# Kernel optimization log

Hardware: AMD Instinct MI355X
Metric: run time of the kernel (lower is better)

The kernel has to match this reference:

```python
import jax, jax.numpy as jnp
import numpy as np

B = 16384
D = 64            # bottom_mlp_layers[-1] = embedding_dim
DENSE = 512
HIST = 50         # history length per row
C_CAMP = 1000     # num_collisions for campaign table (sqrt(1e6))
C_FEAT = 316      # num_collisions for 1e5-vocab tables
NQ_CAMP = 1000    # ceil(1e6/1000)
NQ_FEAT = 317     # ceil(1e5/316)
NFEAT = 7
N = NFEAT + 1 + 1 # sparse features + dense row
PROJ = 128


def setup_inputs() -> dict:
    key = jax.random.key(0)
    ks = jax.random.split(key, 20)
    inp = {
        'x': jax.random.normal(ks[0], (B, DENSE), jnp.float32),
        'hist_idx': jax.random.randint(ks[1], (B * HIST,), 0, 1000000),
        'hist_offsets': jnp.arange(B, dtype=jnp.int64) * HIST,
        'feat_idx': jax.random.randint(ks[2], (B, NFEAT), 0, 100000),
        # QR embedding tables (quotient, remainder)
        'Wq_c': jax.random.normal(ks[3], (NQ_CAMP, D), jnp.float32) * 0.05,
        'Wr_c': jax.random.normal(ks[4], (C_CAMP, D), jnp.float32) * 0.05,
        'Wq_f': jax.random.normal(ks[5], (NFEAT, NQ_FEAT, D), jnp.float32) * 0.05,
        'Wr_f': jax.random.normal(ks[6], (NFEAT, C_FEAT, D), jnp.float32) * 0.05,
        # bottom MLP: 512->512 relu 512->256 relu 256->64
        'W0': jax.random.normal(ks[7], (512, DENSE), jnp.float32) * 0.03,
        'b0': jnp.zeros((512,), jnp.float32),
        'W1': jax.random.normal(ks[8], (256, 512), jnp.float32) * 0.04,
        'b1': jnp.zeros((256,), jnp.float32),
        'W2': jax.random.normal(ks[9], (64, 256), jnp.float32) * 0.06,
        'b2': jnp.zeros((64,), jnp.float32),
        # projection: (D + (N^2-N)/2) -> PROJ ; 64 + 36 = 100
        'Wp': jax.random.normal(ks[10], (PROJ, D + (N * N - N) // 2), jnp.float32) * 0.1,
        'bp': jnp.zeros((PROJ,), jnp.float32),
    }
    return inp


def _forward(x, hist_idx, hist_offsets, feat_idx, Wq_c, Wr_c, Wq_f, Wr_f,
             W0, b0, W1, b1, W2, b2, Wp, bp):
    # bottom MLP
    h = jax.nn.relu(x @ W0.T + b0)
    h = jax.nn.relu(h @ W1.T + b1)
    dense = h @ W2.T + b2                                   # [B, D]

    # QR embedding bag (mode='mean', operation='mult') for history feature
    e = Wq_c[hist_idx // C_CAMP] * Wr_c[hist_idx % C_CAMP]  # [M, D]
    M = hist_idx.shape[0]
    seg = jnp.cumsum(jnp.zeros((M,), jnp.int32).at[hist_offsets].add(1)) - 1
    sums = jax.ops.segment_sum(e, seg, num_segments=B)      # [B, D]
    counts = jnp.diff(jnp.concatenate([hist_offsets, jnp.array([M], hist_offsets.dtype)]))
    hist_emb = sums / counts[:, None].astype(sums.dtype)

    # single-valued QR lookups (bag size 1 -> mean == lookup)
    t = jnp.arange(NFEAT)[None, :]
    fe = Wq_f[t, feat_idx // C_FEAT] * Wr_f[t, feat_idx % C_FEAT]  # [B, NFEAT, D]

    # pairwise dot interaction: upper triangle (offset=1) of T @ T^T
    T = jnp.concatenate([dense[:, None, :], hist_emb[:, None, :], fe], axis=1)  # [B, N, D]
    Z = jnp.einsum('bnd,bmd->bnm', T, T)
    row, col = np.triu_indices(N, k=1)
    Z_flat = Z[:, row, col]                                  # [B, (N^2-N)/2]

    combined = jnp.concatenate([dense, Z_flat], axis=1)
    return combined @ Wp.T + bp                              # [B, PROJ]


def reference(x, hist_idx, hist_offsets, feat_idx, Wq_c, Wr_c, Wq_f, Wr_f,
              W0, b0, W1, b1, W2, b2, Wp, bp):
    return _forward(x, hist_idx, hist_offsets, feat_idx, Wq_c, Wr_c, Wq_f, Wr_f,
                    W0, b0, W1, b1, W2, b2, Wp, bp)
```

## Files before the change

### kernel.cpp

```cpp
#include <hip/hip_runtime.h>
#include <hip/hip_bf16.h>
#include <stdint.h>

#define DENSE_D 512
#define HIDDEN1 512
#define HIDDEN2 256
#define EMB_D   64
#define NFEAT   7
#define NROWS   9
#define NPAIRS  36
#define COMB    100
#define KPROJ   128
#define PROJ    128
#define C_CAMP  1000
#define C_FEAT  316
#define NQ_FEAT 317

typedef __attribute__((ext_vector_type(8))) __bf16 bf16x8;
typedef __attribute__((ext_vector_type(8))) unsigned short ushort8;
typedef __attribute__((ext_vector_type(4))) float  facc4;

#define GLD_LDS16(gp, lp) __builtin_amdgcn_global_load_lds( \
    (__attribute__((address_space(1))) void*)(gp), \
    (__attribute__((address_space(3))) void*)(lp), 16, 0, 0)

__device__ inline unsigned short f2bf(float f) {
    __hip_bfloat16 h = __float2bfloat16(f);
    return *reinterpret_cast<unsigned short*>(&h);
}
__device__ inline float blo(unsigned int u) { return __uint_as_float(u << 16); }
__device__ inline float bhi(unsigned int u) { return __uint_as_float(u & 0xffff0000u); }

template<int BM, int BN, bool RELU, bool OUT_BF16, bool A_F32>
__global__ __launch_bounds__(256)
void gemm_bf16(const void* __restrict__ Avoid,
               const __hip_bfloat16* __restrict__ W,
               const float* __restrict__ bias,
               void* __restrict__ Cout,
               int M, int N, int K)
{
    constexpr int BK   = 32;
    constexpr int MREP = BM / 32;
    constexpr int NREP = BN / 32;
    constexpr int ACH  = BM * BK / 8;
    constexpr int BCH  = BN * BK / 8;

    __shared__ __align__(16) __hip_bfloat16 Asm[BK / 8][BM][8];
    __shared__ __align__(16) __hip_bfloat16 Bsm[BK / 8][BN][8];

    const int tid  = threadIdx.x;
    const int lane = tid & 63;
    const int wave = tid >> 6;
    const int wm   = wave >> 1;
    const int wn   = wave & 1;
    const int row0 = blockIdx.x * BM;
    const int col0 = blockIdx.y * BN;
    const int fr   = lane & 15;
    const int fk   = lane >> 4;

    facc4 acc[MREP][NREP] = {};

    for (int k0 = 0; k0 < K; k0 += BK) {
        if (A_F32) {
            const float* Af = (const float*)Avoid;
            #pragma unroll
            for (int it = 0; it < ACH / 256; ++it) {
                const int p  = it * 256 + tid;
                const int r  = p & (BM - 1);
                const int kc = p / BM;
                const float* src = Af + (size_t)(row0 + r) * K + k0 + kc * 8;
                const float4 v0 = *reinterpret_cast<const float4*>(src);
                const float4 v1 = *reinterpret_cast<const float4*>(src + 4);
                ushort8 cv;
                cv[0] = f2bf(v0.x); cv[1] = f2bf(v0.y);
                cv[2] = f2bf(v0.z); cv[3] = f2bf(v0.w);
                cv[4] = f2bf(v1.x); cv[5] = f2bf(v1.y);
                cv[6] = f2bf(v1.z); cv[7] = f2bf(v1.w);
                *reinterpret_cast<ushort8*>((&Asm[0][0][0]) + (size_t)p * 8) = cv;
            }
        } else {
            const __hip_bfloat16* Ab = (const __hip_bfloat16*)Avoid;
            #pragma unroll
            for (int it = 0; it < ACH / 256; ++it) {
                const int p  = it * 256 + tid;
                const int r  = p & (BM - 1);
                const int kc = p / BM;
                GLD_LDS16(Ab + (size_t)(row0 + r) * K + k0 + kc * 8,
                          (&Asm[0][0][0]) + (size_t)p * 8);
            }
        }
        #pragma unroll
        for (int it = 0; it < BCH / 256; ++it) {
            const int p  = it * 256 + tid;
            const int r  = p & (BN - 1);
            const int kc = p / BN;
            GLD_LDS16(W + (size_t)(col0 + r) * K + k0 + kc * 8,
                      (&Bsm[0][0][0]) + (size_t)p * 8);
        }
        __syncthreads();

        bf16x8 af[MREP], bw[NREP];
        #pragma unroll
        for (int m = 0; m < MREP; ++m)
            af[m] = *reinterpret_cast<const bf16x8*>(
                &Asm[fk][wm * (MREP * 16) + m * 16 + fr][0]);
        #pragma unroll
        for (int n = 0; n < NREP; ++n)
            bw[n] = *reinterpret_cast<const bf16x8*>(
                &Bsm[fk][wn * (NREP * 16) + n * 16 + fr][0]);
        #pragma unroll
        for (int m = 0; m < MREP; ++m)
            #pragma unroll
            for (int n = 0; n < NREP; ++n)
                acc[m][n] = __builtin_amdgcn_mfma_f32_16x16x32_bf16(
                    af[m], bw[n], acc[m][n], 0, 0, 0);
        __syncthreads();
    }

    #pragma unroll
    for (int n = 0; n < NREP; ++n) {
        const int col = col0 + wn * (NREP * 16) + n * 16 + fr;
        const float bv = bias[col];
        #pragma unroll
        for (int m = 0; m < MREP; ++m) {
            #pragma unroll
            for (int j = 0; j < 4; ++j) {
                const int row = row0 + wm * (MREP * 16) + m * 16 + fk * 4 + j;
                float v = acc[m][n][j] + bv;
                if (RELU) v = fmaxf(v, 0.f);
                if (OUT_BF16)
                    ((__hip_bfloat16*)Cout)[(size_t)row * N + col] = __float2bfloat16(v);
                else
                    ((float*)Cout)[(size_t)row * N + col] = v;
            }
        }
    }
}

__device__ inline void cast_seg(const float* __restrict__ src,
                                unsigned short* __restrict__ dst,
                                int n4, int id, int stride)
{
    for (int i = id; i < n4; i += stride) {
        const float4 v = reinterpret_cast<const float4*>(src)[i];
        ushort4 o;
        o.x = f2bf(v.x); o.y = f2bf(v.y); o.z = f2bf(v.z); o.w = f2bf(v.w);
        reinterpret_cast<ushort4*>(dst)[i] = o;
    }
}

__global__ __launch_bounds__(256)
void prep_all(const float* __restrict__ W0, const float* __restrict__ W1,
              const float* __restrict__ W2, const float* __restrict__ Wp,
              const float* __restrict__ Wq_c, const float* __restrict__ Wr_c,
              const float* __restrict__ Wq_f, const float* __restrict__ Wr_f,
              unsigned short* w0b, unsigned short* w1b, unsigned short* w2b,
              unsigned short* wpb, unsigned short* qcb, unsigned short* rcb,
              unsigned short* qfb, unsigned short* rfb)
{
    const int id = blockIdx.x * blockDim.x + threadIdx.x;
    const int stride = gridDim.x * blockDim.x;
    cast_seg(W0,   w0b, HIDDEN1 * DENSE_D / 4, id, stride);
    cast_seg(W1,   w1b, HIDDEN2 * HIDDEN1 / 4, id, stride);
    cast_seg(W2,   w2b, EMB_D * HIDDEN2 / 4,   id, stride);
    cast_seg(Wq_c, qcb, C_CAMP * EMB_D / 4,    id, stride);
    cast_seg(Wr_c, rcb, C_CAMP * EMB_D / 4,    id, stride);
    cast_seg(Wq_f, qfb, NFEAT * NQ_FEAT * EMB_D / 4, id, stride);
    cast_seg(Wr_f, rfb, NFEAT * C_FEAT * EMB_D / 4,  id, stride);
    for (int i = id; i < PROJ * KPROJ; i += stride) {
        const int r = i >> 7, c = i & 127;
        wpb[i] = (c < COMB) ? f2bf(Wp[r * COMB + c]) : (unsigned short)0;
    }
}

__global__ __launch_bounds__(256)
void embed_interact(
    const int* __restrict__ hist_idx, const int* __restrict__ hist_off,
    const int* __restrict__ feat_idx,
    const unsigned short* __restrict__ Wq_cb, const unsigned short* __restrict__ Wr_cb,
    const unsigned short* __restrict__ Wq_fb, const unsigned short* __restrict__ Wr_fb,
    const unsigned short* __restrict__ dense,
    unsigned short* __restrict__ comb, int B, int Mtot)
{
    const int b = blockIdx.x;
    const int t = threadIdx.x;

    __shared__ float T[NROWS][EMB_D + 1];
    __shared__ float part[16][68];
    __shared__ int2  soff[128];
    __shared__ float zf[NPAIRS];

    if (t < 16) {
        const uint2 u = reinterpret_cast<const uint2*>(dense + (size_t)b * EMB_D)[t];
        T[0][t * 4 + 0] = blo(u.x); T[0][t * 4 + 1] = bhi(u.x);
        T[0][t * 4 + 2] = blo(u.y); T[0][t * 4 + 3] = bhi(u.y);
    }
    if (t >= 64 && t < 64 + NFEAT * 16) {
        const int p = t - 64;
        const int f = p >> 4, fd2 = p & 15;
        const int fi = feat_idx[b * NFEAT + f];
        const int q = fi / C_FEAT, r = fi - q * C_FEAT;
        const uint2 qv = *reinterpret_cast<const uint2*>(
            Wq_fb + ((size_t)f * NQ_FEAT + q) * EMB_D + fd2 * 4);
        const uint2 rv = *reinterpret_cast<const uint2*>(
            Wr_fb + ((size_t)f * C_FEAT + r) * EMB_D + fd2 * 4);
        T[2 + f][fd2 * 4 + 0] = blo(qv.x) * blo(rv.x);
        T[2 + f][fd2 * 4 + 1] = bhi(qv.x) * bhi(rv.x);
        T[2 + f][fd2 * 4 + 2] = blo(qv.y) * blo(rv.y);
        T[2 + f][fd2 * 4 + 3] = bhi(qv.y) * bhi(rv.y);
    }

    const int start = hist_off[b];
    const int end   = (b + 1 < B) ? hist_off[b + 1] : Mtot;
    const int cnt   = end - start;
    const int d2 = t & 15;
    const int g  = t >> 4;
    float a0 = 0.f, a1 = 0.f, a2 = 0.f, a3 = 0.f;
    for (int i0 = start; i0 < end; i0 += 128) {
        const int n = min(128, end - i0);
        __syncthreads();
        if (t < n) {
            const int hi = hist_idx[i0 + t];
            const int q = hi / C_CAMP;
            const int r = hi - q * C_CAMP;
            soff[t] = make_int2(q * EMB_D, r * EMB_D);
        }
        __syncthreads();
        for (int i = g; i < n; i += 16) {
            const int2 o = soff[i];
            const uint2 qv = *reinterpret_cast<const uint2*>(Wq_cb + o.x + d2 * 4);
            const uint2 rv = *reinterpret_cast<const uint2*>(Wr_cb + o.y + d2 * 4);
            a0 += blo(qv.x) * blo(rv.x);
            a1 += bhi(qv.x) * bhi(rv.x);
            a2 += blo(qv.y) * blo(rv.y);
            a3 += bhi(qv.y) * bhi(rv.y);
        }
    }
    part[g][d2 * 4 + 0] = a0; part[g][d2 * 4 + 1] = a1;
    part[g][d2 * 4 + 2] = a2; part[g][d2 * 4 + 3] = a3;
    __syncthreads();
    if (t < EMB_D) {
        float s = 0.f;
        #pragma unroll
        for (int gg = 0; gg < 16; ++gg) s += part[gg][t];
        T[1][t] = s / (float)max(cnt, 1);
    }
    __syncthreads();

    if (t < NPAIRS * 4) {
        const int p = t >> 2, sub = t & 3;
        int ii = 0, rem = p;
        while (rem >= (NROWS - 1) - ii) { rem -= (NROWS - 1) - ii; ++ii; }
        const int jj = ii + 1 + rem;
        float s = 0.f;
        const int dbase = sub * 16;
        #pragma unroll
        for (int dd = 0; dd < 16; ++dd) s += T[ii][dbase + dd] * T[jj][dbase + dd];
        s += __shfl_xor(s, 1);
        s += __shfl_xor(s, 2);
        if (sub == 0) zf[p] = s;
    }
    __syncthreads();

    if (t < KPROJ) {
        const float v = (t < EMB_D) ? T[0][t] : (t < COMB ? zf[t - EMB_D] : 0.f);
        comb[(size_t)b * KPROJ + t] = f2bf(v);
    }
}

extern "C" void kernel_launch(void* const* d_in, const int* in_sizes, int n_in,
                              void* d_out, int out_size, void* d_ws, size_t ws_size,
                              hipStream_t stream)
{
    const float* x        = (const float*)d_in[0];
    const int*   hist_idx = (const int*)  d_in[1];
    const int*   hist_off = (const int*)  d_in[2];
    const int*   feat_idx = (const int*)  d_in[3];
    const float* Wq_c     = (const float*)d_in[4];
    const float* Wr_c     = (const float*)d_in[5];
    const float* Wq_f     = (const float*)d_in[6];
    const float* Wr_f     = (const float*)d_in[7];
    const float* W0       = (const float*)d_in[8];
    const float* b0       = (const float*)d_in[9];
    const float* W1       = (const float*)d_in[10];
    const float* b1       = (const float*)d_in[11];
    const float* W2       = (const float*)d_in[12];
    const float* b2       = (const float*)d_in[13];
    const float* Wp       = (const float*)d_in[14];
    const float* bp       = (const float*)d_in[15];

    const int M    = in_sizes[0] / DENSE_D;
    const int Mtot = in_sizes[1];

    char* w = (char*)d_ws;
    auto take = [&](size_t bytes) { char* p = w; w += (bytes + 255) & ~(size_t)255; return p; };
    unsigned short* w0b = (unsigned short*)take(HIDDEN1 * DENSE_D * 2);
    unsigned short* w1b = (unsigned short*)take(HIDDEN2 * HIDDEN1 * 2);
    unsigned short* w2b = (unsigned short*)take(EMB_D * HIDDEN2 * 2);
    unsigned short* wpb = (unsigned short*)take(PROJ * KPROJ * 2);
    unsigned short* qcb = (unsigned short*)take(C_CAMP * EMB_D * 2);
    unsigned short* rcb = (unsigned short*)take(C_CAMP * EMB_D * 2);
    unsigned short* qfb = (unsigned short*)take(NFEAT * NQ_FEAT * EMB_D * 2);
    unsigned short* rfb = (unsigned short*)take(NFEAT * C_FEAT * EMB_D * 2);
    unsigned short* h0b = (unsigned short*)take((size_t)M * HIDDEN1 * 2);
    unsigned short* h1b = (unsigned short*)take((size_t)M * HIDDEN2 * 2);
    unsigned short* dnb = (unsigned short*)take((size_t)M * EMB_D * 2);
    unsigned short* cmb = (unsigned short*)take((size_t)M * KPROJ * 2);

    prep_all<<<512, 256, 0, stream>>>(W0, W1, W2, Wp, Wq_c, Wr_c, Wq_f, Wr_f,
                                      w0b, w1b, w2b, wpb, qcb, rcb, qfb, rfb);

    gemm_bf16<128, 128, true, true, true><<<dim3(M / 128, HIDDEN1 / 128), 256, 0, stream>>>(
        x, (const __hip_bfloat16*)w0b, b0, h0b, M, HIDDEN1, DENSE_D);
    gemm_bf16<128, 64, true, true, false><<<dim3(M / 128, HIDDEN2 / 64), 256, 0, stream>>>(
        h0b, (const __hip_bfloat16*)w1b, b1, h1b, M, HIDDEN2, HIDDEN1);
    gemm_bf16<64, 64, false, true, false><<<dim3(M / 64, EMB_D / 64), 256, 0, stream>>>(
        h1b, (const __hip_bfloat16*)w2b, b2, dnb, M, EMB_D, HIDDEN2);

    embed_interact<<<M, 256, 0, stream>>>(
        hist_idx, hist_off, feat_idx, qcb, rcb, qfb, rfb, dnb, cmb, M, Mtot);

    gemm_bf16<64, 64, false, false, false><<<dim3(M / 64, PROJ / 64), 256, 0, stream>>>(
        cmb, (const __hip_bfloat16*)wpb, bp, (float*)d_out, M, PROJ, KPROJ);
}
```

Baseline: 99.52 us.

## Fuse final MLP layer, embedding bag, interaction and projection into one kernel

Replaces the last bottom-MLP GEMM, the per-row embed_interact kernel and the projection GEMM with a single tail kernel. It handles 32 rows per block, computes the dense layer with MFMA from global memory, gathers the QR embeddings with one thread per row-octet, and computes the pairwise dots and projection through LDS. This removes the intermediate dense and combined buffers, their round trips, and two launches. It also generalises the GEMM template to take a wave layout and retunes the first two GEMMs to larger 512-thread tiles. The interaction inputs are now rounded to bf16 before the dot products, and each thread walks a full history bag serially.

```diff
diff --git a/kernel.cpp b/kernel.cpp
--- a/kernel.cpp
+++ b/kernel.cpp
@@ -31,19 +31,20 @@
 __device__ inline float blo(unsigned int u) { return __uint_as_float(u << 16); }
 __device__ inline float bhi(unsigned int u) { return __uint_as_float(u & 0xffff0000u); }
 
-template<int BM, int BN, bool RELU, bool OUT_BF16, bool A_F32>
-__global__ __launch_bounds__(256)
+template<int BM, int BN, int WM, int WN, bool RELU, bool OUT_BF16, bool A_F32>
+__global__ __launch_bounds__(WM * WN * 64)
 void gemm_bf16(const void* __restrict__ Avoid,
                const __hip_bfloat16* __restrict__ W,
                const float* __restrict__ bias,
                void* __restrict__ Cout,
                int M, int N, int K)
 {
-    constexpr int BK   = 32;
-    constexpr int MREP = BM / 32;
-    constexpr int NREP = BN / 32;
-    constexpr int ACH  = BM * BK / 8;
-    constexpr int BCH  = BN * BK / 8;
+    constexpr int BK      = 32;
+    constexpr int THREADS = WM * WN * 64;
+    constexpr int MREP    = BM / (WM * 16);
+    constexpr int NREP    = BN / (WN * 16);
+    constexpr int ACH     = BM * BK / 8;
+    constexpr int BCH     = BN * BK / 8;
 
     __shared__ __align__(16) __hip_bfloat16 Asm[BK / 8][BM][8];
     __shared__ __align__(16) __hip_bfloat16 Bsm[BK / 8][BN][8];
@@ -51,8 +52,8 @@
     const int tid  = threadIdx.x;
     const int lane = tid & 63;
     const int wave = tid >> 6;
-    const int wm   = wave >> 1;
-    const int wn   = wave & 1;
+    const int wm   = wave / WN;
+    const int wn   = wave % WN;
     const int row0 = blockIdx.x * BM;
     const int col0 = blockIdx.y * BN;
     const int fr   = lane & 15;
@@ -63,9 +64,7 @@
     for (int k0 = 0; k0 < K; k0 += BK) {
         if (A_F32) {
             const float* Af = (const float*)Avoid;
-            #pragma unroll
-            for (int it = 0; it < ACH / 256; ++it) {
-                const int p  = it * 256 + tid;
+            for (int p = tid; p < ACH; p += THREADS) {
                 const int r  = p & (BM - 1);
                 const int kc = p / BM;
                 const float* src = Af + (size_t)(row0 + r) * K + k0 + kc * 8;
@@ -76,22 +75,19 @@
                 cv[2] = f2bf(v0.z); cv[3] = f2bf(v0.w);
                 cv[4] = f2bf(v1.x); cv[5] = f2bf(v1.y);
                 cv[6] = f2bf(v1.z); cv[7] = f2bf(v1.w);
-                *reinterpret_cast<ushort8*>((&Asm[0][0][0]) + (size_t)p * 8) = cv;
+                *reinterpret_cast<ushort8*>(
+                    (unsigned short*)(&Asm[0][0][0]) + (size_t)p * 8) = cv;
             }
         } else {
             const __hip_bfloat16* Ab = (const __hip_bfloat16*)Avoid;
-            #pragma unroll
-            for (int it = 0; it < ACH / 256; ++it) {
-                const int p  = it * 256 + tid;
+            for (int p = tid; p < ACH; p += THREADS) {
                 const int r  = p & (BM - 1);
                 const int kc = p / BM;
                 GLD_LDS16(Ab + (size_t)(row0 + r) * K + k0 + kc * 8,
                           (&Asm[0][0][0]) + (size_t)p * 8);
             }
         }
-        #pragma unroll
-        for (int it = 0; it < BCH / 256; ++it) {
-            const int p  = it * 256 + tid;
+        for (int p = tid; p < BCH; p += THREADS) {
             const int r  = p & (BN - 1);
             const int kc = p / BN;
             GLD_LDS16(W + (size_t)(col0 + r) * K + k0 + kc * 8,
@@ -174,97 +170,166 @@
 }
 
 __global__ __launch_bounds__(256)
-void embed_interact(
-    const int* __restrict__ hist_idx, const int* __restrict__ hist_off,
-    const int* __restrict__ feat_idx,
-    const unsigned short* __restrict__ Wq_cb, const unsigned short* __restrict__ Wr_cb,
-    const unsigned short* __restrict__ Wq_fb, const unsigned short* __restrict__ Wr_fb,
-    const unsigned short* __restrict__ dense,
-    unsigned short* __restrict__ comb, int B, int Mtot)
-{
-    const int b = blockIdx.x;
-    const int t = threadIdx.x;
-
-    __shared__ float T[NROWS][EMB_D + 1];
-    __shared__ float part[16][68];
-    __shared__ int2  soff[128];
-    __shared__ float zf[NPAIRS];
-
-    if (t < 16) {
-        const uint2 u = reinterpret_cast<const uint2*>(dense + (size_t)b * EMB_D)[t];
-        T[0][t * 4 + 0] = blo(u.x); T[0][t * 4 + 1] = bhi(u.x);
-        T[0][t * 4 + 2] = blo(u.y); T[0][t * 4 + 3] = bhi(u.y);
-    }
-    if (t >= 64 && t < 64 + NFEAT * 16) {
-        const int p = t - 64;
-        const int f = p >> 4, fd2 = p & 15;
-        const int fi = feat_idx[b * NFEAT + f];
-        const int q = fi / C_FEAT, r = fi - q * C_FEAT;
-        const uint2 qv = *reinterpret_cast<const uint2*>(
-            Wq_fb + ((size_t)f * NQ_FEAT + q) * EMB_D + fd2 * 4);
-        const uint2 rv = *reinterpret_cast<const uint2*>(
-            Wr_fb + ((size_t)f * C_FEAT + r) * EMB_D + fd2 * 4);
-        T[2 + f][fd2 * 4 + 0] = blo(qv.x) * blo(rv.x);
-        T[2 + f][fd2 * 4 + 1] = bhi(qv.x) * bhi(rv.x);
-        T[2 + f][fd2 * 4 + 2] = blo(qv.y) * blo(rv.y);
-        T[2 + f][fd2 * 4 + 3] = bhi(qv.y) * bhi(rv.y);
-    }
-
-    const int start = hist_off[b];
-    const int end   = (b + 1 < B) ? hist_off[b + 1] : Mtot;
-    const int cnt   = end - start;
-    const int d2 = t & 15;
-    const int g  = t >> 4;
-    float a0 = 0.f, a1 = 0.f, a2 = 0.f, a3 = 0.f;
-    for (int i0 = start; i0 < end; i0 += 128) {
-        const int n = min(128, end - i0);
-        __syncthreads();
-        if (t < n) {
-            const int hi = hist_idx[i0 + t];
-            const int q = hi / C_CAMP;
-            const int r = hi - q * C_CAMP;
-            soff[t] = make_int2(q * EMB_D, r * EMB_D);
-        }
-        __syncthreads();
-        for (int i = g; i < n; i += 16) {
-            const int2 o = soff[i];
-            const uint2 qv = *reinterpret_cast<const uint2*>(Wq_cb + o.x + d2 * 4);
-            const uint2 rv = *reinterpret_cast<const uint2*>(Wr_cb + o.y + d2 * 4);
-            a0 += blo(qv.x) * blo(rv.x);
-            a1 += bhi(qv.x) * bhi(rv.x);
-            a2 += blo(qv.y) * blo(rv.y);
-            a3 += bhi(qv.y) * bhi(rv.y);
-        }
-    }
-    part[g][d2 * 4 + 0] = a0; part[g][d2 * 4 + 1] = a1;
-    part[g][d2 * 4 + 2] = a2; part[g][d2 * 4 + 3] = a3;
+void tail_fused(const unsigned short* __restrict__ h1b,
+                const unsigned short* __restrict__ w2b,
+                const float* __restrict__ b2,
+                const int* __restrict__ hist_idx,
+                const int* __restrict__ hist_off,
+                const int* __restrict__ feat_idx,
+                const unsigned short* __restrict__ qcb,
+                const unsigned short* __restrict__ rcb,
+                const unsigned short* __restrict__ qfb,
+                const unsigned short* __restrict__ rfb,
+                const unsigned short* __restrict__ wpb,
+                const float* __restrict__ bp,
+                float* __restrict__ out,
+                int B, int Mtot)
+{
+    const int r0   = blockIdx.x * 32;
+    const int t    = threadIdx.x;
+    const int lane = t & 63;
+    const int wave = t >> 6;
+    const int wm   = wave >> 1;
+    const int wn   = wave & 1;
+    const int fr   = lane & 15;
+    const int fk   = lane >> 4;
+
+    __shared__ unsigned short T[32][NROWS][68];
+    __shared__ unsigned short combs[32][136];
+
+    {
+        facc4 acc[2] = {};
+        const unsigned short* arow = h1b + (size_t)(r0 + wm * 16 + fr) * HIDDEN2;
+        #pragma unroll
+        for (int kw = 0; kw < 8; ++kw) {
+            const bf16x8 af = *reinterpret_cast<const bf16x8*>(arow + kw * 32 + fk * 8);
+            #pragma unroll
+            for (int n = 0; n < 2; ++n) {
+                const bf16x8 bw = *reinterpret_cast<const bf16x8*>(
+                    w2b + (size_t)(wn * 32 + n * 16 + fr) * HIDDEN2 + kw * 32 + fk * 8);
+                acc[n] = __builtin_amdgcn_mfma_f32_16x16x32_bf16(af, bw, acc[n], 0, 0, 0);
+            }
+        }
+        #pragma unroll
+        for (int n = 0; n < 2; ++n) {
+            const int col = wn * 32 + n * 16 + fr;
+            const float bv = b2[col];
+            #pragma unroll
+            for (int j = 0; j < 4; ++j) {
+                const int row = wm * 16 + fk * 4 + j;
+                const unsigned short hv = f2bf(acc[n][j] + bv);
+                T[row][0][col]  = hv;
+                combs[row][col] = hv;
+            }
+        }
+    }
+
+    for (int p = t; p < 32 * 18; p += 256) {
+        const int row = p / 18, c = p % 18;
+        *reinterpret_cast<unsigned int*>(&combs[row][100 + c * 2]) = 0u;
+    }
+
+    {
+        const int row = t >> 3;
+        const int oc  = t & 7;
+        const int br  = r0 + row;
+
+        const int fbase = br * NFEAT;
+        #pragma unroll
+        for (int f = 0; f < NFEAT; ++f) {
+            const int fi = feat_idx[fbase + f];
+            const int q = fi / C_FEAT, r = fi - q * C_FEAT;
+            const unsigned short* qp = qfb + ((size_t)f * NQ_FEAT + q) * EMB_D + oc * 8;
+            const unsigned short* rp = rfb + ((size_t)f * C_FEAT  + r) * EMB_D + oc * 8;
+            const uint2 qa = *reinterpret_cast<const uint2*>(qp);
+            const uint2 qb = *reinterpret_cast<const uint2*>(qp + 4);
+            const uint2 ra = *reinterpret_cast<const uint2*>(rp);
+            const uint2 rb = *reinterpret_cast<const uint2*>(rp + 4);
+            union { ushort8 v; uint2 u[2]; } pk;
+            pk.v[0] = f2bf(blo(qa.x) * blo(ra.x));
+            pk.v[1] = f2bf(bhi(qa.x) * bhi(ra.x));
+            pk.v[2] = f2bf(blo(qa.y) * blo(ra.y));
+            pk.v[3] = f2bf(bhi(qa.y) * bhi(ra.y));
+            pk.v[4] = f2bf(blo(qb.x) * blo(rb.x));
+            pk.v[5] = f2bf(bhi(qb.x) * bhi(rb.x));
+            pk.v[6] = f2bf(blo(qb.y) * blo(rb.y));
+            pk.v[7] = f2bf(bhi(qb.y) * bhi(rb.y));
+            *reinterpret_cast<uint2*>(&T[row][2 + f][oc * 8])     = pk.u[0];
+            *reinterpret_cast<uint2*>(&T[row][2 + f][oc * 8 + 4]) = pk.u[1];
+        }
+
+        const int start = hist_off[br];
+        const int end   = (br + 1 < B) ? hist_off[br + 1] : Mtot;
+        const int cnt   = end - start;
+        const int* hp = hist_idx + start;
+        float a[8] = {};
+        #pragma unroll 2
+        for (int i = 0; i < cnt; ++i) {
+            const int hi = hp[i];
+            const int q = hi / C_CAMP, r = hi - q * C_CAMP;
+            const unsigned short* qp = qcb + (size_t)q * EMB_D + oc * 8;
+            const unsigned short* rp = rcb + (size_t)r * EMB_D + oc * 8;
+            const uint2 qa = *reinterpret_cast<const uint2*>(qp);
+            const uint2 qb = *reinterpret_cast<const uint2*>(qp + 4);
+            const uint2 ra = *reinterpret_cast<const uint2*>(rp);
+            const uint2 rb = *reinterpret_cast<const uint2*>(rp + 4);
+            a[0] += blo(qa.x) * blo(ra.x); a[1] += bhi(qa.x) * bhi(ra.x);
+            a[2] += blo(qa.y) * blo(ra.y); a[3] += bhi(qa.y) * bhi(ra.y);
+            a[4] += blo(qb.x) * blo(rb.x); a[5] += bhi(qb.x) * bhi(rb.x);
+            a[6] += blo(qb.y) * blo(rb.y); a[7] += bhi(qb.y) * bhi(rb.y);
+        }
+        const float inv = 1.f / (float)max(cnt, 1);
+        union { ushort8 v; uint2 u[2]; } pk;
+        #pragma unroll
+        for (int k = 0; k < 8; ++k) pk.v[k] = f2bf(a[k] * inv);
+        *reinterpret_cast<uint2*>(&T[row][1][oc * 8])     = pk.u[0];
+        *reinterpret_cast<uint2*>(&T[row][1][oc * 8 + 4]) = pk.u[1];
+    }
     __syncthreads();
-    if (t < EMB_D) {
+
+    for (int p = t; p < NPAIRS * 32; p += 256) {
+        const int row = p & 31;
+        const int pr  = p >> 5;
+        int i = 0, rem = pr;
+        while (rem >= (NROWS - 1) - i) { rem -= (NROWS - 1) - i; ++i; }
+        const int j = i + 1 + rem;
+        const unsigned short* ti = &T[row][i][0];
+        const unsigned short* tj = &T[row][j][0];
         float s = 0.f;
         #pragma unroll
-        for (int gg = 0; gg < 16; ++gg) s += part[gg][t];
-        T[1][t] = s / (float)max(cnt, 1);
+        for (int d = 0; d < EMB_D; d += 4) {
+            const uint2 u = *reinterpret_cast<const uint2*>(ti + d);
+            const uint2 v = *reinterpret_cast<const uint2*>(tj + d);
+            s += blo(u.x) * blo(v.x) + bhi(u.x) * bhi(v.x)
+               + blo(u.y) * blo(v.y) + bhi(u.y) * bhi(v.y);
+        }
+        combs[row][EMB_D + pr] = f2bf(s);
     }
     __syncthreads();
 
-    if (t < NPAIRS * 4) {
-        const int p = t >> 2, sub = t & 3;
-        int ii = 0, rem = p;
-        while (rem >= (NROWS - 1) - ii) { rem -= (NROWS - 1) - ii; ++ii; }
-        const int jj = ii + 1 + rem;
-        float s = 0.f;
-        const int dbase = sub * 16;
-        #pragma unroll
-        for (int dd = 0; dd < 16; ++dd) s += T[ii][dbase + dd] * T[jj][dbase + dd];
-        s += __shfl_xor(s, 1);
-        s += __shfl_xor(s, 2);
-        if (sub == 0) zf[p] = s;
-    }
-    __syncthreads();
-
-    if (t < KPROJ) {
-        const float v = (t < EMB_D) ? T[0][t] : (t < COMB ? zf[t - EMB_D] : 0.f);
-        comb[(size_t)b * KPROJ + t] = f2bf(v);
+    {
+        facc4 acc[4] = {};
+        #pragma unroll
+        for (int kw = 0; kw < 4; ++kw) {
+            const bf16x8 af = *reinterpret_cast<const bf16x8*>(
+                &combs[wm * 16 + fr][kw * 32 + fk * 8]);
+            #pragma unroll
+            for (int n = 0; n < 4; ++n) {
+                const bf16x8 bw = *reinterpret_cast<const bf16x8*>(
+                    wpb + (size_t)(wn * 64 + n * 16 + fr) * KPROJ + kw * 32 + fk * 8);
+                acc[n] = __builtin_amdgcn_mfma_f32_16x16x32_bf16(af, bw, acc[n], 0, 0, 0);
+            }
+        }
+        #pragma unroll
+        for (int n = 0; n < 4; ++n) {
+            const int col = wn * 64 + n * 16 + fr;
+            const float bv = bp[col];
+            #pragma unroll
+            for (int j = 0; j < 4; ++j) {
+                const int row = wm * 16 + fk * 4 + j;
+                out[(size_t)(r0 + row) * PROJ + col] = acc[n][j] + bv;
+            }
+        }
     }
 }
 
@@ -304,22 +369,19 @@
     unsigned short* rfb = (unsigned short*)take(NFEAT * C_FEAT * EMB_D * 2);
     unsigned short* h0b = (unsigned short*)take((size_t)M * HIDDEN1 * 2);
     unsigned short* h1b = (unsigned short*)take((size_t)M * HIDDEN2 * 2);
-    unsigned short* dnb = (unsigned short*)take((size_t)M * EMB_D * 2);
-    unsigned short* cmb = (unsigned short*)take((size_t)M * KPROJ * 2);
 
     prep_all<<<512, 256, 0, stream>>>(W0, W1, W2, Wp, Wq_c, Wr_c, Wq_f, Wr_f,
                                       w0b, w1b, w2b, wpb, qcb, rcb, qfb, rfb);
 
-    gemm_bf16<128, 128, true, true, true><<<dim3(M / 128, HIDDEN1 / 128), 256, 0, stream>>>(
+    gemm_bf16<128, 256, 2, 4, true, true, true>
+        <<<dim3(M / 128, HIDDEN1 / 256), 512, 0, stream>>>(
         x, (const __hip_bfloat16*)w0b, b0, h0b, M, HIDDEN1, DENSE_D);
-    gemm_bf16<128, 64, true, true, false><<<dim3(M / 128, HIDDEN2 / 64), 256, 0, stream>>>(
+
+    gemm_bf16<64, 256, 2, 4, true, true, false>
+        <<<dim3(M / 64, HIDDEN2 / 256), 512, 0, stream>>>(
         h0b, (const __hip_bfloat16*)w1b, b1, h1b, M, HIDDEN2, HIDDEN1);
-    gemm_bf16<64, 64, false, true, false><<<dim3(M / 64, EMB_D / 64), 256, 0, stream>>>(
-        h1b, (const __hip_bfloat16*)w2b, b2, dnb, M, EMB_D, HIDDEN2);
-
-    embed_interact<<<M, 256, 0, stream>>>(
-        hist_idx, hist_off, feat_idx, qcb, rcb, qfb, rfb, dnb, cmb, M, Mtot);
-
-    gemm_bf16<64, 64, false, false, false><<<dim3(M / 64, PROJ / 64), 256, 0, stream>>>(
-        cmb, (const __hip_bfloat16*)wpb, bp, (float*)d_out, M, PROJ, KPROJ);
-}
+
+    tail_fused<<<M / 32, 256, 0, stream>>>(
+        h1b, w2b, b2, hist_idx, hist_off, feat_idx,
+        qcb, rcb, qfb, rfb, wpb, bp, (float*)d_out, M, Mtot);
+}
```

Measured after the change: 87.67 us. 11.9% less time.
